# Kernel tuning notes

Hardware: AMD Instinct MI355X
Metric: run time of the kernel (lower is better)

## Reference

```python
import jax, jax.numpy as jnp
import numpy as np

HUBER_DELTA = 1.0
SMOOTH_L1_BETA = 1.0 / 9
WEIGHT_NONZERO = 1.5
WEIGHT_ZERO = 0.6


def _huber(pred, target, delta=HUBER_DELTA):
    err = jnp.abs(pred - target)
    quad = jnp.clip(err, 0.0, delta)
    lin = err - quad
    return 0.5 * quad ** 2 + delta * lin


def _smooth_l1(pred, gt, beta=SMOOTH_L1_BETA):
    l1 = jnp.abs(pred - gt)
    return jnp.where(l1 < beta, 0.5 * l1 ** 2 / beta, l1 - 0.5 * beta)


def _softargmax_points(x):
    # x: [B, C, D, H, W] -> points [B, C, 3] (softmax over whole volume,
    # coordinate grids (i+1)/dim, then coord*dim - 1, matching the torch code)
    B, C, D, H, W = x.shape
    p = jax.nn.softmax(x.reshape(B, C, D * H * W), axis=-1).reshape(B, C, D, H, W)
    gx = (jnp.arange(D, dtype=x.dtype) + 1.0) / D
    gy = (jnp.arange(H, dtype=x.dtype) + 1.0) / H
    gz = (jnp.arange(W, dtype=x.dtype) + 1.0) / W
    cx = jnp.einsum('bcdhw,d->bc', p, gx) * D - 1.0
    cy = jnp.einsum('bcdhw,h->bc', p, gy) * H - 1.0
    cz = jnp.einsum('bcdhw,w->bc', p, gz) * W - 1.0
    return jnp.stack([cx, cy, cz], axis=-1)


def _heatmap_loss(pred, gt):
    basic = _huber(pred, gt)
    weights = jnp.where(gt != 0, WEIGHT_NONZERO, WEIGHT_ZERO)
    per_sample = jnp.sum(weights * basic, axis=(2, 3, 4))  # [B, C]
    return jnp.mean(per_sample)


def _offset_loss(pred, gt):
    B, C = pred.shape[0], pred.shape[1]
    # torch version uses .item() -> coordinates are constants w.r.t. autograd
    pp = jax.lax.stop_gradient(_softargmax_points(pred))
    gp = jax.lax.stop_gradient(_softargmax_points(gt))
    return jnp.sum(_smooth_l1(pp, gp)) / (B * C)


def setup_inputs() -> dict:
    key = jax.random.key(0)
    k1, k2 = jax.random.split(key)
    shape = (2, 8, 64, 128, 128)
    pred = jax.random.normal(k1, shape, dtype=jnp.float32)
    gt = jax.random.normal(k2, shape, dtype=jnp.float32)
    return {"pred": pred, "gt": gt}


def reference(pred, gt):
    heatmap_loss = _heatmap_loss(pred, gt) * 1.0
    offset_loss = _offset_loss(pred, gt) * 1.0
    loss = heatmap_loss + offset_loss / jax.lax.stop_gradient(offset_loss / heatmap_loss)
    return loss
```

## Files before the change

kernel.cpp:

```cpp
#include <hip/hip_runtime.h>


typedef float f4 __attribute__((ext_vector_type(4)));

__device__ __forceinline__ float hterm(float p, float g) {
    float err  = fabsf(p - g);
    float quad = fminf(err, 1.0f);
    float lin  = err - quad;
    float h    = 0.5f * quad * quad + lin;
    float w    = (g != 0.0f) ? 1.5f : 0.6f;
    return w * h;
}

__device__ __forceinline__ float hterm4(f4 p, f4 g) {
    return hterm(p.x, g.x) + hterm(p.y, g.y) + hterm(p.z, g.z) + hterm(p.w, g.w);
}

#define PER_THREAD 8

__global__ __launch_bounds__(256) void heatmap_reduce_kernel(
        const f4* __restrict__ pred,
        const f4* __restrict__ gt,
        float* __restrict__ partial, int stride) {
    const int tid = blockIdx.x * 256 + threadIdx.x;

    f4 p[PER_THREAD], g[PER_THREAD];
    #pragma unroll
    for (int j = 0; j < PER_THREAD; ++j)
        p[j] = __builtin_nontemporal_load(&pred[tid + j * stride]);
    #pragma unroll
    for (int j = 0; j < PER_THREAD; ++j)
        g[j] = __builtin_nontemporal_load(&gt[tid + j * stride]);

    float acc = 0.0f;
    #pragma unroll
    for (int j = 0; j < PER_THREAD; ++j)
        acc += hterm4(p[j], g[j]);

    #pragma unroll
    for (int off = 32; off > 0; off >>= 1)
        acc += __shfl_down(acc, off, 64);

    __shared__ float wsum[4];
    int lane = threadIdx.x & 63;
    int wave = threadIdx.x >> 6;
    if (lane == 0) wsum[wave] = acc;
    __syncthreads();

    if (threadIdx.x == 0)
        partial[blockIdx.x] = wsum[0] + wsum[1] + wsum[2] + wsum[3];
}

__global__ __launch_bounds__(256) void finalize_kernel(
        const float* __restrict__ partial, float* __restrict__ out, int nblocks) {
    float s = 0.0f;
    for (int i = threadIdx.x; i < nblocks; i += 256)
        s += partial[i];

    #pragma unroll
    for (int off = 32; off > 0; off >>= 1)
        s += __shfl_down(s, off, 64);

    __shared__ float wsum[4];
    int lane = threadIdx.x & 63;
    int wave = threadIdx.x >> 6;
    if (lane == 0) wsum[wave] = s;
    __syncthreads();

    if (threadIdx.x == 0)
        out[0] = (wsum[0] + wsum[1] + wsum[2] + wsum[3]) * 0.125f;
}

extern "C" void kernel_launch(void* const* d_in, const int* in_sizes, int n_in,
                              void* d_out, int out_size, void* d_ws, size_t ws_size,
                              hipStream_t stream) {
    const float* pred = (const float*)d_in[0];
    const float* gt   = (const float*)d_in[1];
    float* out     = (float*)d_out;
    float* partial = (float*)d_ws;

    int n  = in_sizes[0];
    int n4 = n >> 2;

    const int block  = 256;
    const int grid   = n4 / (block * PER_THREAD);
    const int stride = grid * block;

    heatmap_reduce_kernel<<<grid, block, 0, stream>>>(
        (const f4*)pred, (const f4*)gt, partial, stride);

    finalize_kernel<<<1, block, 0, stream>>>(partial, out, grid);
}
```

Before: 146.3 us.

## Stream heatmap inputs through LDS with global_load_lds in a fixed grid

Replaces direct nontemporal register loads with `__builtin_amdgcn_global_load_lds` DMA into shared memory. A fixed grid of 1024 blocks each walks 8 contiguous chunks of 512 float4 per input, with a barrier before and after each chunk. The aim is to skip VGPR staging and get contiguous per-block access. In exchange, each thread keeps far fewer loads in flight and pays two barriers per chunk, which can cut memory-level parallelism. The problem size is now hardcoded through GRID rather than read from `in_sizes`.

```diff
diff --git a/kernel.cpp b/kernel.cpp
--- a/kernel.cpp
+++ b/kernel.cpp
@@ -16,38 +16,53 @@
     return hterm(p.x, g.x) + hterm(p.y, g.y) + hterm(p.z, g.z) + hterm(p.w, g.w);
 }
 
-#define PER_THREAD 8
+#define CHUNK_F4 512
+#define NITER    8
+#define GRID     1024
 
 __global__ __launch_bounds__(256) void heatmap_reduce_kernel(
         const f4* __restrict__ pred,
         const f4* __restrict__ gt,
-        float* __restrict__ partial, int stride) {
-    const int tid = blockIdx.x * 256 + threadIdx.x;
+        float* __restrict__ partial) {
+    __shared__ f4 lds_pred[CHUNK_F4];
+    __shared__ f4 lds_gt[CHUNK_F4];
 
-    f4 p[PER_THREAD], g[PER_THREAD];
-    #pragma unroll
-    for (int j = 0; j < PER_THREAD; ++j)
-        p[j] = __builtin_nontemporal_load(&pred[tid + j * stride]);
-    #pragma unroll
-    for (int j = 0; j < PER_THREAD; ++j)
-        g[j] = __builtin_nontemporal_load(&gt[tid + j * stride]);
+    const int t    = threadIdx.x;
+    const int wave = t >> 6;
+    const int lane = t & 63;
+    const int base = blockIdx.x * (CHUNK_F4 * NITER);
 
     float acc = 0.0f;
-    #pragma unroll
-    for (int j = 0; j < PER_THREAD; ++j)
-        acc += hterm4(p[j], g[j]);
+    for (int it = 0; it < NITER; ++it) {
+        const int chunk = base + it * CHUNK_F4;
+        #pragma unroll
+        for (int k = 0; k < 2; ++k) {
+            const int idx = wave * 128 + k * 64;
+            __builtin_amdgcn_global_load_lds(
+                (const __attribute__((address_space(1))) void*)&pred[chunk + idx + lane],
+                (__attribute__((address_space(3))) void*)&lds_pred[idx],
+                16, 0, 0);
+            __builtin_amdgcn_global_load_lds(
+                (const __attribute__((address_space(1))) void*)&gt[chunk + idx + lane],
+                (__attribute__((address_space(3))) void*)&lds_gt[idx],
+                16, 0, 0);
+        }
+        __syncthreads();
+        #pragma unroll
+        for (int k = 0; k < 2; ++k)
+            acc += hterm4(lds_pred[t + k * 256], lds_gt[t + k * 256]);
+        __syncthreads();
+    }
 
     #pragma unroll
     for (int off = 32; off > 0; off >>= 1)
         acc += __shfl_down(acc, off, 64);
 
     __shared__ float wsum[4];
-    int lane = threadIdx.x & 63;
-    int wave = threadIdx.x >> 6;
     if (lane == 0) wsum[wave] = acc;
     __syncthreads();
 
-    if (threadIdx.x == 0)
+    if (t == 0)
         partial[blockIdx.x] = wsum[0] + wsum[1] + wsum[2] + wsum[3];
 }
 
@@ -79,15 +94,8 @@
     float* out     = (float*)d_out;
     float* partial = (float*)d_ws;
 
-    int n  = in_sizes[0];
-    int n4 = n >> 2;
+    heatmap_reduce_kernel<<<GRID, 256, 0, stream>>>(
+        (const f4*)pred, (const f4*)gt, partial);
 
-    const int block  = 256;
-    const int grid   = n4 / (block * PER_THREAD);
-    const int stride = grid * block;
-
-    heatmap_reduce_kernel<<<grid, block, 0, stream>>>(
-        (const f4*)pred, (const f4*)gt, partial, stride);
-
-    finalize_kernel<<<1, block, 0, stream>>>(partial, out, grid);
+    finalize_kernel<<<1, 256, 0, stream>>>(partial, out, GRID);
 }
```

Result: no change. 147.6 us (+1.0%).
